# Optimization experiments

Hardware: AMD Instinct MI355X
Metric: run time of the kernel (lower is better)

## Reference

```python
import jax, jax.numpy as jnp
import numpy as np

KERNEL_SIZE = 5
GROUP_SIZE = 1
SCALE_FACTOR = 2


def setup_inputs() -> dict:
    key = jax.random.key(0)
    k1, k2 = jax.random.split(key)
    N, C, H, W = 8, 128, 64, 64
    s = SCALE_FACTOR
    features = jax.random.normal(k1, (N, C, H, W), dtype=jnp.float32)
    # content-aware reassembly kernels at output resolution (typically softmax-normalized upstream)
    masks = jax.random.uniform(k2, (N, GROUP_SIZE * KERNEL_SIZE * KERNEL_SIZE, H * s, W * s), dtype=jnp.float32)
    return {"features": features, "masks": masks}


def reference(features, masks):
    """CARAFE forward.

    out[n, c, ho, wo] = sum_{i,j} features[n, c, ho//s + i - pad, wo//s + j - pad]
                                  * masks[n, g*k^2 + (i*k+j), ho, wo],  g = c // (C/G)
    with zero padding outside the feature map.
    """
    k, G, s = KERNEL_SIZE, GROUP_SIZE, SCALE_FACTOR
    N, C, H, W = features.shape
    pad = (k - 1) // 2
    Cg = C // G

    fp = jnp.pad(features, ((0, 0), (0, 0), (pad, pad), (pad, pad)))
    # gather the k*k shifted neighborhoods: (N, C, k^2, H, W)
    patches = jnp.stack(
        [fp[:, :, i:i + H, j:j + W] for i in range(k) for j in range(k)], axis=2
    )
    P = patches.reshape(N, G, Cg, k * k, H, W)
    # masks at output resolution, factored as (low-res pixel h,w) x (sub-pixel p,q)
    M = masks.reshape(N, G, k * k, H, s, W, s)
    # per-pixel, per-group weighted sum over the k^2 neighborhood
    out = jnp.einsum('ngcKhw,ngKhpwq->ngchpwq', P, M)
    return out.reshape(N, C, H * s, W * s)
```

## Files before the change

kernel.cpp:

```cpp
#include <hip/hip_runtime.h>


#define KK 5
#define PAD 2
#define CIN 128
#define HH 64
#define WW 64
#define HO 128
#define WO 128
#define CH_PER_BLOCK 16
#define CH_PER_WAVE 8
#define LDS_STRIDE 68

__global__ __launch_bounds__(128, 4)
void carafe_fwd(const float* __restrict__ feat,
                const float* __restrict__ masks,
                float* __restrict__ out) {
    __shared__ float lds[CH_PER_BLOCK][KK][LDS_STRIDE];

    const int tid  = threadIdx.x;
    const int lane = tid & 63;
    const int sub  = tid >> 6;
    const int h    = blockIdx.x;
    const int c0   = blockIdx.y * CH_PER_BLOCK;
    const int n    = blockIdx.z;

    float2 m[KK * KK][2];
    const float* mbase = masks + (size_t)n * (KK * KK) * HO * WO
                               + (size_t)(2 * h) * WO + 2 * lane;
    #pragma unroll
    for (int k = 0; k < KK * KK; ++k) {
        m[k][0] = *(const float2*)(mbase + (size_t)k * HO * WO);
        m[k][1] = *(const float2*)(mbase + (size_t)k * HO * WO + WO);
    }

    for (int it = tid; it < CH_PER_BLOCK * KK * 2; it += 128) {
        int rowid = it >> 1;
        int side  = it & 1;
        float* dst = &lds[0][0][0] + rowid * LDS_STRIDE + side * (LDS_STRIDE - 2);
        *(float2*)dst = make_float2(0.f, 0.f);
    }

    const float* fnc = feat + ((size_t)n * CIN + c0) * HH * WW;
    #pragma unroll
    for (int t = 0; t < 20; ++t) {
        int idx = t * 128 + tid;
        int ch  = idx / 160;
        int rem = idx - ch * 160;
        int r   = rem >> 5;
        int c2  = rem & 31;
        int rr  = h - PAD + r;
        bool ok = (unsigned)rr < (unsigned)HH;
        int rc  = ok ? rr : 0;
        float2 v = *(const float2*)(fnc + ((size_t)ch * HH + rc) * WW + 2 * c2);
        if (!ok) v = make_float2(0.f, 0.f);
        *(float2*)(&lds[ch][r][2 + 2 * c2]) = v;
    }
    __syncthreads();

    const int chb = sub * CH_PER_WAVE;
    float* obase = out + ((size_t)n * CIN + c0 + chb) * HO * WO
                       + (size_t)(2 * h) * WO + 2 * lane;

    #pragma unroll
    for (int cc = 0; cc < CH_PER_WAVE; ++cc) {
        float2 a0 = make_float2(0.f, 0.f);
        float2 a1 = make_float2(0.f, 0.f);

        #pragma unroll
        for (int i = 0; i < KK; ++i) {
            const float* row = &lds[chb + cc][i][lane];
            float f[KK];
            #pragma unroll
            for (int j = 0; j < KK; ++j) f[j] = row[j];
            #pragma unroll
            for (int j = 0; j < KK; ++j) {
                const float2 m0 = m[i * KK + j][0];
                const float2 m1 = m[i * KK + j][1];
                a0.x += f[j] * m0.x;  a0.y += f[j] * m0.y;
                a1.x += f[j] * m1.x;  a1.y += f[j] * m1.y;
            }
        }

        float* o = obase + (size_t)cc * HO * WO;
        *(float2*)(o)      = a0;
        *(float2*)(o + WO) = a1;
    }
}

extern "C" void kernel_launch(void* const* d_in, const int* in_sizes, int n_in,
                              void* d_out, int out_size, void* d_ws, size_t ws_size,
                              hipStream_t stream) {
    const float* feat  = (const float*)d_in[0];
    const float* masks = (const float*)d_in[1];
    float* out = (float*)d_out;

    dim3 grid(HH, CIN / CH_PER_BLOCK, 8);
    dim3 block(128);
    carafe_fwd<<<grid, block, 0, stream>>>(feat, masks, out);
}
```

Before: 115.5 us.

## Split output sub-rows across waves and widen feature loads to float4

Doubles the block to 256 threads so each wave handles one of the two output sub-rows, which halves the per-thread mask registers and accumulators. The LDS stride grows to 72 and the feature tile is staged with float4 loads, with the data offset by 4 for alignment. An empty asm pin keeps the mask registers live. The aim is more waves in flight to hide memory latency, at the cost of redundant LDS reads of features across the paired waves.

```diff
diff --git a/kernel.cpp b/kernel.cpp
--- a/kernel.cpp
+++ b/kernel.cpp
@@ -10,9 +10,9 @@
 #define WO 128
 #define CH_PER_BLOCK 16
 #define CH_PER_WAVE 8
-#define LDS_STRIDE 68
+#define LDS_STRIDE 72
 
-__global__ __launch_bounds__(128, 4)
+__global__ __launch_bounds__(256, 4)
 void carafe_fwd(const float* __restrict__ feat,
                 const float* __restrict__ masks,
                 float* __restrict__ out) {
@@ -20,71 +20,76 @@
 
     const int tid  = threadIdx.x;
     const int lane = tid & 63;
-    const int sub  = tid >> 6;
+    const int wid  = tid >> 6;
+    const int p    = wid & 1;
+    const int sub  = wid >> 1;
     const int h    = blockIdx.x;
     const int c0   = blockIdx.y * CH_PER_BLOCK;
     const int n    = blockIdx.z;
+    const int ho   = 2 * h + p;
 
-    float2 m[KK * KK][2];
+    float2 m[KK * KK];
     const float* mbase = masks + (size_t)n * (KK * KK) * HO * WO
-                               + (size_t)(2 * h) * WO + 2 * lane;
+                               + (size_t)ho * WO + 2 * lane;
     #pragma unroll
     for (int k = 0; k < KK * KK; ++k) {
-        m[k][0] = *(const float2*)(mbase + (size_t)k * HO * WO);
-        m[k][1] = *(const float2*)(mbase + (size_t)k * HO * WO + WO);
+        m[k] = *(const float2*)(mbase + (size_t)k * HO * WO);
+    }
+    #pragma unroll
+    for (int k = 0; k < KK * KK; ++k) {
+        asm volatile("" : "+v"(m[k].x), "+v"(m[k].y));
     }
 
-    for (int it = tid; it < CH_PER_BLOCK * KK * 2; it += 128) {
-        int rowid = it >> 1;
-        int side  = it & 1;
-        float* dst = &lds[0][0][0] + rowid * LDS_STRIDE + side * (LDS_STRIDE - 2);
-        *(float2*)dst = make_float2(0.f, 0.f);
+    {
+        int it = tid;
+        if (it < CH_PER_BLOCK * KK * 2) {
+            int rowid = it >> 1;
+            int side  = it & 1;
+            float* dst = &lds[0][0][0] + rowid * LDS_STRIDE + 2 + side * 66;
+            *(float2*)dst = make_float2(0.f, 0.f);
+        }
     }
 
     const float* fnc = feat + ((size_t)n * CIN + c0) * HH * WW;
     #pragma unroll
-    for (int t = 0; t < 20; ++t) {
-        int idx = t * 128 + tid;
-        int ch  = idx / 160;
-        int rem = idx - ch * 160;
-        int r   = rem >> 5;
-        int c2  = rem & 31;
+    for (int t = 0; t < 5; ++t) {
+        int idx = t * 256 + tid;
+        int ch  = idx / 80;
+        int rem = idx - ch * 80;
+        int r   = rem >> 4;
+        int c4  = rem & 15;
         int rr  = h - PAD + r;
         bool ok = (unsigned)rr < (unsigned)HH;
         int rc  = ok ? rr : 0;
-        float2 v = *(const float2*)(fnc + ((size_t)ch * HH + rc) * WW + 2 * c2);
-        if (!ok) v = make_float2(0.f, 0.f);
-        *(float2*)(&lds[ch][r][2 + 2 * c2]) = v;
+        float4 v = *(const float4*)(fnc + ((size_t)ch * HH + rc) * WW + 4 * c4);
+        if (!ok) v = make_float4(0.f, 0.f, 0.f, 0.f);
+        *(float4*)(&lds[ch][r][4 + 4 * c4]) = v;
     }
     __syncthreads();
 
     const int chb = sub * CH_PER_WAVE;
     float* obase = out + ((size_t)n * CIN + c0 + chb) * HO * WO
-                       + (size_t)(2 * h) * WO + 2 * lane;
+                       + (size_t)ho * WO + 2 * lane;
 
     #pragma unroll
     for (int cc = 0; cc < CH_PER_WAVE; ++cc) {
-        float2 a0 = make_float2(0.f, 0.f);
-        float2 a1 = make_float2(0.f, 0.f);
+        float2 acc = make_float2(0.f, 0.f);
 
         #pragma unroll
         for (int i = 0; i < KK; ++i) {
-            const float* row = &lds[chb + cc][i][lane];
+            const float* row = &lds[chb + cc][i][2 + lane];
             float f[KK];
             #pragma unroll
             for (int j = 0; j < KK; ++j) f[j] = row[j];
             #pragma unroll
             for (int j = 0; j < KK; ++j) {
-                const float2 m0 = m[i * KK + j][0];
-                const float2 m1 = m[i * KK + j][1];
-                a0.x += f[j] * m0.x;  a0.y += f[j] * m0.y;
-                a1.x += f[j] * m1.x;  a1.y += f[j] * m1.y;
+                const float2 mk = m[i * KK + j];
+                acc.x += f[j] * mk.x;
+                acc.y += f[j] * mk.y;
             }
         }
 
-        float* o = obase + (size_t)cc * HO * WO;
-        *(float2*)(o)      = a0;
-        *(float2*)(o + WO) = a1;
+        *(float2*)(obase + (size_t)cc * HO * WO) = acc;
     }
 }
 
@@ -96,6 +101,6 @@
     float* out = (float*)d_out;
 
     dim3 grid(HH, CIN / CH_PER_BLOCK, 8);
-    dim3 block(128);
+    dim3 block(256);
     carafe_fwd<<<grid, block, 0, stream>>>(feat, masks, out);
 }
```

Result: faster. 108.7 us (-5.9%).
